# Performance work log

Measured on AMD Instinct MI355X. Metric: run time of the kernel, lower is better.

Reference implementation:

```python
import jax, jax.numpy as jnp
import numpy as np

B, S, D, H = 2, 2048, 768, 12
HD = D // H  # 64
SCALE = jnp.sqrt(jnp.float32(D / H))  # sqrt(head_dim) = 8


def setup_inputs() -> dict:
    key = jax.random.key(0)
    ks = jax.random.split(key, 11)
    s = 1.0 / np.sqrt(D)
    inp = {
        'Q': jax.random.normal(ks[0], (B, S, D), jnp.float32),
        'K': jax.random.normal(ks[1], (B, S, D), jnp.float32),
        'V': jax.random.normal(ks[2], (B, S, D), jnp.float32),
        # True = masked out (causal upper triangle), broadcast over heads
        'mask': jnp.broadcast_to(jnp.triu(jnp.ones((S, S), bool), k=1)[None, None], (B, 1, S, S)),
        'Wq': jax.random.uniform(ks[3], (D, D), jnp.float32, -s, s),
        'bq': jax.random.uniform(ks[4], (D,), jnp.float32, -s, s),
        'Wk': jax.random.uniform(ks[5], (D, D), jnp.float32, -s, s),
        'bk': jax.random.uniform(ks[6], (D,), jnp.float32, -s, s),
        'Wv': jax.random.uniform(ks[7], (D, D), jnp.float32, -s, s),
        'bv': jax.random.uniform(ks[8], (D,), jnp.float32, -s, s),
        'Wo': jax.random.uniform(ks[9], (D, D), jnp.float32, -s, s),
        'bo': jax.random.uniform(ks[10], (D,), jnp.float32, -s, s),
    }
    return inp


def _split_heads(x):  # [B,S,D] -> [B,H,S,HD]
    return x.reshape(B, S, H, HD).transpose(0, 2, 1, 3)


def reference(Q, K, V, mask, Wq, bq, Wk, bk, Wv, bv, Wo, bo):
    q = _split_heads(Q @ Wq.T + bq)
    k = _split_heads(K @ Wk.T + bk)
    v = _split_heads(V @ Wv.T + bv)
    # [B,H,S,S] attention scores
    scores = jnp.einsum('bhqd,bhkd->bhqk', q, k) / SCALE
    scores = jnp.where(mask, jnp.float32(-1e9), scores)
    weights = jax.nn.softmax(scores, axis=-1)
    attn = jnp.einsum('bhqk,bhkd->bhqd', weights, v)
    x = attn.transpose(0, 2, 1, 3).reshape(B, S, D)
    x = x @ Wo.T + bo
    return x, weights
```

## Files before the change

### kernel.cpp

```cpp
#include <hip/hip_runtime.h>

#define S_LEN 2048
#define DMODEL 768
#define NHEAD 12
#define BATCH 2
#define X_ELEMS ((size_t)BATCH * S_LEN * DMODEL)
#define W_ELEMS ((size_t)BATCH * NHEAD * S_LEN * S_LEN)
#define WMAT_ELEMS ((size_t)DMODEL * DMODEL)

typedef __attribute__((ext_vector_type(8))) short bf16x8;
typedef __attribute__((ext_vector_type(4))) float f32x4;

__device__ __forceinline__ unsigned short f2bf(float f) {
    union { float f; unsigned int u; } v; v.f = f;
    unsigned int u = v.u;
    return (unsigned short)((u + 0x7FFFu + ((u >> 16) & 1u)) >> 16);
}

__device__ __forceinline__ bf16x8 pack8(float4 a, float4 b) {
    bf16x8 r;
    r[0] = (short)f2bf(a.x); r[1] = (short)f2bf(a.y);
    r[2] = (short)f2bf(a.z); r[3] = (short)f2bf(a.w);
    r[4] = (short)f2bf(b.x); r[5] = (short)f2bf(b.y);
    r[6] = (short)f2bf(b.z); r[7] = (short)f2bf(b.w);
    return r;
}

__device__ __forceinline__ float rmax16(float v) {
    v = fmaxf(v, __shfl_xor(v, 1));
    v = fmaxf(v, __shfl_xor(v, 2));
    v = fmaxf(v, __shfl_xor(v, 4));
    v = fmaxf(v, __shfl_xor(v, 8));
    return v;
}
__device__ __forceinline__ float rsum16(float v) {
    v += __shfl_xor(v, 1); v += __shfl_xor(v, 2);
    v += __shfl_xor(v, 4); v += __shfl_xor(v, 8);
    return v;
}

struct ConvArgs {
    const float* src[7];
    unsigned short* dst[7];
    int n[7];
};

__global__ __launch_bounds__(256) void convert_kernel(ConvArgs a) {
    int t = blockIdx.y;
    int idx = (blockIdx.x * 256 + threadIdx.x) * 8;
    if (idx >= a.n[t]) return;
    const float4* s = (const float4*)(a.src[t] + idx);
    float4 lo = s[0], hi = s[1];
    *(bf16x8*)(a.dst[t] + idx) = pack8(lo, hi);
}

__global__ __launch_bounds__(256) void gemm_kernel(
    const unsigned short* __restrict__ A, const unsigned short* __restrict__ Bw,
    const float* __restrict__ bias, unsigned short* __restrict__ outb,
    float* __restrict__ outf, int mode, float oscale)
{
    __shared__ unsigned short As[128 * 40];
    __shared__ unsigned short Bs[128 * 40];
    int tid = threadIdx.x;
    int bm = blockIdx.x & 31, bn = blockIdx.x >> 5;
    int m0 = bm * 128, n0 = bn * 128;
    int wid = tid >> 6, l = tid & 63;
    int wr = wid >> 1, wc = wid & 1;
    int lr = l & 15, ks = l >> 4, g = l >> 4;

    int srow = tid >> 1, scg = (tid & 1) * 16;
    const unsigned short* aptr = A + (size_t)(m0 + srow) * DMODEL + scg;
    const unsigned short* bptr = Bw + (size_t)(n0 + srow) * DMODEL + scg;
    unsigned short* adst = &As[srow * 40 + scg];
    unsigned short* bdst = &Bs[srow * 40 + scg];

    bf16x8 ar0 = *(const bf16x8*)aptr, ar1 = *(const bf16x8*)(aptr + 8);
    bf16x8 br0 = *(const bf16x8*)bptr, br1 = *(const bf16x8*)(bptr + 8);

    f32x4 acc[4][4];
#pragma unroll
    for (int mi = 0; mi < 4; ++mi)
#pragma unroll
        for (int ni = 0; ni < 4; ++ni) acc[mi][ni] = (f32x4){0.f, 0.f, 0.f, 0.f};

    for (int kk = 0; kk < 24; ++kk) {
        __syncthreads();
        *(bf16x8*)adst = ar0; *(bf16x8*)(adst + 8) = ar1;
        *(bf16x8*)bdst = br0; *(bf16x8*)(bdst + 8) = br1;
        __syncthreads();
        if (kk < 23) {
            int k0 = (kk + 1) * 32;
            ar0 = *(const bf16x8*)(aptr + k0); ar1 = *(const bf16x8*)(aptr + k0 + 8);
            br0 = *(const bf16x8*)(bptr + k0); br1 = *(const bf16x8*)(bptr + k0 + 8);
        }
        bf16x8 af[4], bf_[4];
#pragma unroll
        for (int mi = 0; mi < 4; ++mi)
            af[mi] = *(const bf16x8*)&As[(wr * 64 + mi * 16 + lr) * 40 + ks * 8];
#pragma unroll
        for (int ni = 0; ni < 4; ++ni)
            bf_[ni] = *(const bf16x8*)&Bs[(wc * 64 + ni * 16 + lr) * 40 + ks * 8];
#pragma unroll
        for (int mi = 0; mi < 4; ++mi)
#pragma unroll
            for (int ni = 0; ni < 4; ++ni)
                acc[mi][ni] = __builtin_amdgcn_mfma_f32_16x16x32_bf16(af[mi], bf_[ni], acc[mi][ni], 0, 0, 0);
    }

#pragma unroll
    for (int mi = 0; mi < 4; ++mi)
#pragma unroll
        for (int ni = 0; ni < 4; ++ni) {
            int ngl = n0 + wc * 64 + ni * 16 + lr;
            float bv = bias[ngl];
            int h = ngl >> 6, d = ngl & 63;
#pragma unroll
            for (int i = 0; i < 4; ++i) {
                int mg = m0 + wr * 64 + mi * 16 + g * 4 + i;
                float val = (acc[mi][ni][i] + bv) * oscale;
                if (mode == 0) {
                    int b = mg >> 11, s = mg & 2047;
                    outb[((size_t)(b * NHEAD + h) * S_LEN + s) * 64 + d] = f2bf(val);
                } else if (mode == 1) {
                    int b = mg >> 11, s = mg & 2047;
                    outb[((size_t)(b * NHEAD + h) * 64 + d) * S_LEN + s] = f2bf(val);
                } else {
                    outf[(size_t)mg * DMODEL + ngl] = val;
                }
            }
        }
}

__global__ __launch_bounds__(256) void zero_upper_kernel(float* __restrict__ wts) {
    int qblk = blockIdx.x >> 5, tcol = blockIdx.x & 31;
    if (tcol <= qblk) return;
    int bh = blockIdx.y;
    int tid = threadIdx.x;
    float4 z = {0.f, 0.f, 0.f, 0.f};
    float* base = wts + ((size_t)bh * S_LEN + qblk * 64) * S_LEN + tcol * 64;
#pragma unroll
    for (int it = 0; it < 4; ++it) {
        int r = it * 16 + (tid >> 4);
        *(float4*)&base[(size_t)r * S_LEN + (tid & 15) * 4] = z;
    }
}

__global__ __launch_bounds__(256) void attn_fused_kernel(
    const unsigned short* __restrict__ qbuf, const unsigned short* __restrict__ kbuf,
    const unsigned short* __restrict__ vTbuf, float* __restrict__ wts,
    unsigned short* __restrict__ abuf)
{
    __shared__ unsigned short kt[64 * 72];
    __shared__ unsigned short vt[64 * 72];
    __shared__ unsigned short pt[128 * 72];
    int tid = threadIdx.x;
    int wid = tid >> 6, l = tid & 63;
    int qblk = 15 - blockIdx.x;
    int bh = blockIdx.y;
    int qb0 = qblk * 128;
    int qr0 = qb0 + wid * 32;
    int lr = l & 15, ks = l >> 4, g = l >> 4;
    int nt = 2 * qblk + 2;
    int tmaxw = (qr0 + 31) >> 6;

    const unsigned short* ksrc = kbuf + (size_t)bh * S_LEN * 64;
    const unsigned short* vsrc = vTbuf + (size_t)bh * 64 * S_LEN;

    bf16x8 qf[2][2];
#pragma unroll
    for (int mi = 0; mi < 2; ++mi) {
        const unsigned short* qp = qbuf + ((size_t)bh * S_LEN + qr0 + mi * 16 + lr) * 64 + ks * 8;
        qf[mi][0] = *(const bf16x8*)qp;
        qf[mi][1] = *(const bf16x8*)(qp + 32);
    }

    int srow = tid >> 2, sgrp = (tid & 3) * 16;
    const unsigned short* kstage = ksrc + (size_t)srow * 64 + sgrp;
    const unsigned short* vstage = vsrc + (size_t)srow * S_LEN + sgrp;
    unsigned short* kdst = &kt[srow * 72 + sgrp];
    unsigned short* vdst = &vt[srow * 72 + sgrp];
    unsigned short* ptw = &pt[(wid * 32) * 72];

    float m[2][4], lsum[2][4];
#pragma unroll
    for (int mi = 0; mi < 2; ++mi)
#pragma unroll
        for (int i = 0; i < 4; ++i) { m[mi][i] = -1e30f; lsum[mi][i] = 0.f; }

    bf16x8 kr0 = *(const bf16x8*)kstage;
    bf16x8 kr1 = *(const bf16x8*)(kstage + 8);
    for (int t = 0; t < nt; ++t) {
        __syncthreads();
        *(bf16x8*)kdst = kr0; *(bf16x8*)(kdst + 8) = kr1;
        __syncthreads();
        if (t + 1 < nt) {
            kr0 = *(const bf16x8*)(kstage + (size_t)(t + 1) * 4096);
            kr1 = *(const bf16x8*)(kstage + (size_t)(t + 1) * 4096 + 8);
        }
        if (t > tmaxw) continue;
        f32x4 accs[2][4];
#pragma unroll
        for (int c = 0; c < 4; ++c) {
            bf16x8 kf0 = *(const bf16x8*)&kt[(c * 16 + lr) * 72 + ks * 8];
            bf16x8 kf1 = *(const bf16x8*)&kt[(c * 16 + lr) * 72 + 32 + ks * 8];
#pragma unroll
            for (int mi = 0; mi < 2; ++mi) {
                f32x4 a = {0.f, 0.f, 0.f, 0.f};
                a = __builtin_amdgcn_mfma_f32_16x16x32_bf16(qf[mi][0], kf0, a, 0, 0, 0);
                a = __builtin_amdgcn_mfma_f32_16x16x32_bf16(qf[mi][1], kf1, a, 0, 0, 0);
                accs[mi][c] = a;
            }
        }
        if (t == tmaxw) {
#pragma unroll
            for (int c = 0; c < 4; ++c) {
                int kcol = t * 64 + c * 16 + lr;
#pragma unroll
                for (int mi = 0; mi < 2; ++mi)
#pragma unroll
                    for (int i = 0; i < 4; ++i)
                        if (kcol > qr0 + mi * 16 + g * 4 + i) accs[mi][c][i] = -1e30f;
            }
        }
#pragma unroll
        for (int mi = 0; mi < 2; ++mi)
#pragma unroll
            for (int i = 0; i < 4; ++i) {
                float a0 = accs[mi][0][i], a1 = accs[mi][1][i];
                float a2 = accs[mi][2][i], a3 = accs[mi][3][i];
                float tm = fmaxf(fmaxf(a0, a1), fmaxf(a2, a3));
                float mn = fmaxf(m[mi][i], tm);
                float ls = lsum[mi][i] * __expf(m[mi][i] - mn);
                float p0 = __expf(a0 - mn); if (a0 < -5e29f) p0 = 0.f;
                float p1 = __expf(a1 - mn); if (a1 < -5e29f) p1 = 0.f;
                float p2 = __expf(a2 - mn); if (a2 < -5e29f) p2 = 0.f;
                float p3 = __expf(a3 - mn); if (a3 < -5e29f) p3 = 0.f;
                lsum[mi][i] = ls + (p0 + p1) + (p2 + p3);
                m[mi][i] = mn;
            }
    }

    float invl[2][4];
#pragma unroll
    for (int mi = 0; mi < 2; ++mi)
#pragma unroll
        for (int i = 0; i < 4; ++i) {
            float mf = rmax16(m[mi][i]);
            float ls = lsum[mi][i] * __expf(m[mi][i] - mf);
            ls = rsum16(ls);
            invl[mi][i] = 1.0f / ls;
            m[mi][i] = mf;
        }

    f32x4 oacc[2][4];
#pragma unroll
    for (int mi = 0; mi < 2; ++mi)
#pragma unroll
        for (int dt = 0; dt < 4; ++dt) oacc[mi][dt] = (f32x4){0.f, 0.f, 0.f, 0.f};

    kr0 = *(const bf16x8*)kstage;
    kr1 = *(const bf16x8*)(kstage + 8);
    bf16x8 vr0 = *(const bf16x8*)vstage;
    bf16x8 vr1 = *(const bf16x8*)(vstage + 8);
    for (int t = 0; t < nt; ++t) {
        __syncthreads();
        *(bf16x8*)kdst = kr0; *(bf16x8*)(kdst + 8) = kr1;
        *(bf16x8*)vdst = vr0; *(bf16x8*)(vdst + 8) = vr1;
        __syncthreads();
        if (t + 1 < nt) {
            kr0 = *(const bf16x8*)(kstage + (size_t)(t + 1) * 4096);
            kr1 = *(const bf16x8*)(kstage + (size_t)(t + 1) * 4096 + 8);
            vr0 = *(const bf16x8*)(vstage + (t + 1) * 64);
            vr1 = *(const bf16x8*)(vstage + (t + 1) * 64 + 8);
        }
        if (t > tmaxw) continue;
        f32x4 accs[2][4];
#pragma unroll
        for (int c = 0; c < 4; ++c) {
            bf16x8 kf0 = *(const bf16x8*)&kt[(c * 16 + lr) * 72 + ks * 8];
            bf16x8 kf1 = *(const bf16x8*)&kt[(c * 16 + lr) * 72 + 32 + ks * 8];
#pragma unroll
            for (int mi = 0; mi < 2; ++mi) {
                f32x4 a = {0.f, 0.f, 0.f, 0.f};
                a = __builtin_amdgcn_mfma_f32_16x16x32_bf16(qf[mi][0], kf0, a, 0, 0, 0);
                a = __builtin_amdgcn_mfma_f32_16x16x32_bf16(qf[mi][1], kf1, a, 0, 0, 0);
                accs[mi][c] = a;
            }
        }
        if (t == tmaxw) {
#pragma unroll
            for (int c = 0; c < 4; ++c) {
                int kcol = t * 64 + c * 16 + lr;
#pragma unroll
                for (int mi = 0; mi < 2; ++mi)
#pragma unroll
                    for (int i = 0; i < 4; ++i)
                        if (kcol > qr0 + mi * 16 + g * 4 + i) accs[mi][c][i] = -1e30f;
            }
        }
#pragma unroll
        for (int c = 0; c < 4; ++c) {
            int kcol = t * 64 + c * 16 + lr;
#pragma unroll
            for (int mi = 0; mi < 2; ++mi)
#pragma unroll
                for (int i = 0; i < 4; ++i) {
                    int qrow = qr0 + mi * 16 + g * 4 + i;
                    float w = __expf(accs[mi][c][i] - m[mi][i]) * invl[mi][i];
                    wts[((size_t)bh * S_LEN + qrow) * S_LEN + kcol] = w;
                    ptw[(mi * 16 + g * 4 + i) * 72 + c * 16 + lr] = f2bf(w);
                }
        }
        bf16x8 pa[2][2];
#pragma unroll
        for (int mi = 0; mi < 2; ++mi) {
            pa[mi][0] = *(const bf16x8*)&ptw[(mi * 16 + lr) * 72 + ks * 8];
            pa[mi][1] = *(const bf16x8*)&ptw[(mi * 16 + lr) * 72 + 32 + ks * 8];
        }
#pragma unroll
        for (int dt = 0; dt < 4; ++dt) {
            bf16x8 vb0 = *(const bf16x8*)&vt[(dt * 16 + lr) * 72 + ks * 8];
            bf16x8 vb1 = *(const bf16x8*)&vt[(dt * 16 + lr) * 72 + 32 + ks * 8];
#pragma unroll
            for (int mi = 0; mi < 2; ++mi) {
                oacc[mi][dt] = __builtin_amdgcn_mfma_f32_16x16x32_bf16(pa[mi][0], vb0, oacc[mi][dt], 0, 0, 0);
                oacc[mi][dt] = __builtin_amdgcn_mfma_f32_16x16x32_bf16(pa[mi][1], vb1, oacc[mi][dt], 0, 0, 0);
            }
        }
    }

    int b = bh / NHEAD, h = bh % NHEAD;
#pragma unroll
    for (int mi = 0; mi < 2; ++mi)
#pragma unroll
        for (int dt = 0; dt < 4; ++dt)
#pragma unroll
            for (int i = 0; i < 4; ++i) {
                int s = qr0 + mi * 16 + g * 4 + i;
                abuf[(((size_t)b * S_LEN + s) * NHEAD + h) * 64 + dt * 16 + lr] = f2bf(oacc[mi][dt][i]);
            }
}

extern "C" void kernel_launch(void* const* d_in, const int* in_sizes, int n_in,
                              void* d_out, int out_size, void* d_ws, size_t ws_size,
                              hipStream_t stream) {
    const float* Q  = (const float*)d_in[0];
    const float* K  = (const float*)d_in[1];
    const float* V  = (const float*)d_in[2];
    const float* Wq = (const float*)d_in[4];
    const float* bq = (const float*)d_in[5];
    const float* Wk = (const float*)d_in[6];
    const float* bk = (const float*)d_in[7];
    const float* Wv = (const float*)d_in[8];
    const float* bv = (const float*)d_in[9];
    const float* Wo = (const float*)d_in[10];
    const float* bo = (const float*)d_in[11];

    float* xout = (float*)d_out;
    float* wts  = xout + X_ELEMS;

    unsigned short* p = (unsigned short*)d_ws;
    unsigned short* Qb   = p; p += X_ELEMS;
    unsigned short* Kb   = p; p += X_ELEMS;
    unsigned short* Vb   = p; p += X_ELEMS;
    unsigned short* Wqb  = p; p += WMAT_ELEMS;
    unsigned short* Wkb  = p; p += WMAT_ELEMS;
    unsigned short* Wvb  = p; p += WMAT_ELEMS;
    unsigned short* Wob  = p; p += WMAT_ELEMS;
    unsigned short* qbuf = p; p += X_ELEMS;
    unsigned short* kbuf = p; p += X_ELEMS;
    unsigned short* vT   = p; p += X_ELEMS;
    unsigned short* abuf = p; p += X_ELEMS;

    ConvArgs ca;
    ca.src[0] = Q;  ca.dst[0] = Qb;  ca.n[0] = (int)X_ELEMS;
    ca.src[1] = K;  ca.dst[1] = Kb;  ca.n[1] = (int)X_ELEMS;
    ca.src[2] = V;  ca.dst[2] = Vb;  ca.n[2] = (int)X_ELEMS;
    ca.src[3] = Wq; ca.dst[3] = Wqb; ca.n[3] = (int)WMAT_ELEMS;
    ca.src[4] = Wk; ca.dst[4] = Wkb; ca.n[4] = (int)WMAT_ELEMS;
    ca.src[5] = Wv; ca.dst[5] = Wvb; ca.n[5] = (int)WMAT_ELEMS;
    ca.src[6] = Wo; ca.dst[6] = Wob; ca.n[6] = (int)WMAT_ELEMS;
    convert_kernel<<<dim3(1536, 7), 256, 0, stream>>>(ca);

    const int GEMM_GRID = 32 * 6;
    gemm_kernel<<<GEMM_GRID, 256, 0, stream>>>(Qb, Wqb, bq, qbuf, nullptr, 0, 0.125f);
    gemm_kernel<<<GEMM_GRID, 256, 0, stream>>>(Kb, Wkb, bk, kbuf, nullptr, 0, 1.0f);
    gemm_kernel<<<GEMM_GRID, 256, 0, stream>>>(Vb, Wvb, bv, vT,   nullptr, 1, 1.0f);

    zero_upper_kernel<<<dim3(32 * 32, 24), 256, 0, stream>>>(wts);

    attn_fused_kernel<<<dim3(16, 24), 256, 0, stream>>>(qbuf, kbuf, vT, wts, abuf);

    gemm_kernel<<<GEMM_GRID, 256, 0, stream>>>(abuf, Wob, bo, nullptr, xout, 2, 1.0f);
}
```

Before: 672.3 us.

## Batch QKV projections, fold zeroing into single-wave attention, use exp2

Merges the three projection GEMMs into one launch indexed by blockIdx.y. The attention kernel becomes a one-wave 32-row block that reads K and V straight from global memory with no LDS staging and no barriers. It also zeroes its own upper-triangle weight tiles, which removes the separate zero kernel. Softmax uses the hardware exp2 instruction, with log2(e) folded into the Q projection scale and -inf masking. Together these cut launch count, sync overhead and idle waves, at the cost of losing K/V reuse across waves and relying more on cache bandwidth.

```diff
diff --git a/kernel.cpp b/kernel.cpp
--- a/kernel.cpp
+++ b/kernel.cpp
@@ -11,6 +11,8 @@
 typedef __attribute__((ext_vector_type(8))) short bf16x8;
 typedef __attribute__((ext_vector_type(4))) float f32x4;
 
+#define NEG_INF (-__builtin_inff())
+
 __device__ __forceinline__ unsigned short f2bf(float f) {
     union { float f; unsigned int u; } v; v.f = f;
     unsigned int u = v.u;
@@ -26,6 +28,10 @@
     return r;
 }
 
+__device__ __forceinline__ float exp2_hw(float x) {
+    float r; asm("v_exp_f32 %0, %1" : "=v"(r) : "v"(x)); return r;
+}
+
 __device__ __forceinline__ float rmax16(float v) {
     v = fmaxf(v, __shfl_xor(v, 1));
     v = fmaxf(v, __shfl_xor(v, 2));
@@ -54,7 +60,7 @@
     *(bf16x8*)(a.dst[t] + idx) = pack8(lo, hi);
 }
 
-__global__ __launch_bounds__(256) void gemm_kernel(
+__device__ __forceinline__ void gemm_core(
     const unsigned short* __restrict__ A, const unsigned short* __restrict__ Bw,
     const float* __restrict__ bias, unsigned short* __restrict__ outb,
     float* __restrict__ outf, int mode, float oscale)
@@ -131,40 +137,44 @@
         }
 }
 
-__global__ __launch_bounds__(256) void zero_upper_kernel(float* __restrict__ wts) {
-    int qblk = blockIdx.x >> 5, tcol = blockIdx.x & 31;
-    if (tcol <= qblk) return;
-    int bh = blockIdx.y;
-    int tid = threadIdx.x;
-    float4 z = {0.f, 0.f, 0.f, 0.f};
-    float* base = wts + ((size_t)bh * S_LEN + qblk * 64) * S_LEN + tcol * 64;
-#pragma unroll
-    for (int it = 0; it < 4; ++it) {
-        int r = it * 16 + (tid >> 4);
-        *(float4*)&base[(size_t)r * S_LEN + (tid & 15) * 4] = z;
-    }
-}
-
-__global__ __launch_bounds__(256) void attn_fused_kernel(
+struct ProjArgs {
+    const unsigned short* A[3];
+    const unsigned short* W[3];
+    const float* bias[3];
+    unsigned short* out[3];
+    int mode[3];
+    float scale[3];
+};
+
+__global__ __launch_bounds__(256) void proj3_kernel(ProjArgs p) {
+    int z = blockIdx.y;
+    gemm_core(p.A[z], p.W[z], p.bias[z], p.out[z], nullptr, p.mode[z], p.scale[z]);
+}
+
+__global__ __launch_bounds__(256) void gemm_kernel(
+    const unsigned short* __restrict__ A, const unsigned short* __restrict__ Bw,
+    const float* __restrict__ bias, unsigned short* __restrict__ outb,
+    float* __restrict__ outf, int mode, float oscale)
+{
+    gemm_core(A, Bw, bias, outb, outf, mode, oscale);
+}
+
+__global__ __launch_bounds__(64) void attn_kernel(
     const unsigned short* __restrict__ qbuf, const unsigned short* __restrict__ kbuf,
     const unsigned short* __restrict__ vTbuf, float* __restrict__ wts,
     unsigned short* __restrict__ abuf)
 {
-    __shared__ unsigned short kt[64 * 72];
-    __shared__ unsigned short vt[64 * 72];
-    __shared__ unsigned short pt[128 * 72];
-    int tid = threadIdx.x;
-    int wid = tid >> 6, l = tid & 63;
-    int qblk = 15 - blockIdx.x;
+    __shared__ unsigned short pt[32 * 72];
+    int l = threadIdx.x;
+    int chunk = 63 - (int)blockIdx.x;
     int bh = blockIdx.y;
-    int qb0 = qblk * 128;
-    int qr0 = qb0 + wid * 32;
+    int qr0 = chunk * 32;
     int lr = l & 15, ks = l >> 4, g = l >> 4;
-    int nt = 2 * qblk + 2;
-    int tmaxw = (qr0 + 31) >> 6;
+    int tdiag = qr0 >> 6;
 
     const unsigned short* ksrc = kbuf + (size_t)bh * S_LEN * 64;
     const unsigned short* vsrc = vTbuf + (size_t)bh * 64 * S_LEN;
+    float* wbh = wts + (size_t)bh * S_LEN * S_LEN;
 
     bf16x8 qf[2][2];
 #pragma unroll
@@ -174,35 +184,19 @@
         qf[mi][1] = *(const bf16x8*)(qp + 32);
     }
 
-    int srow = tid >> 2, sgrp = (tid & 3) * 16;
-    const unsigned short* kstage = ksrc + (size_t)srow * 64 + sgrp;
-    const unsigned short* vstage = vsrc + (size_t)srow * S_LEN + sgrp;
-    unsigned short* kdst = &kt[srow * 72 + sgrp];
-    unsigned short* vdst = &vt[srow * 72 + sgrp];
-    unsigned short* ptw = &pt[(wid * 32) * 72];
-
     float m[2][4], lsum[2][4];
 #pragma unroll
     for (int mi = 0; mi < 2; ++mi)
 #pragma unroll
-        for (int i = 0; i < 4; ++i) { m[mi][i] = -1e30f; lsum[mi][i] = 0.f; }
-
-    bf16x8 kr0 = *(const bf16x8*)kstage;
-    bf16x8 kr1 = *(const bf16x8*)(kstage + 8);
-    for (int t = 0; t < nt; ++t) {
-        __syncthreads();
-        *(bf16x8*)kdst = kr0; *(bf16x8*)(kdst + 8) = kr1;
-        __syncthreads();
-        if (t + 1 < nt) {
-            kr0 = *(const bf16x8*)(kstage + (size_t)(t + 1) * 4096);
-            kr1 = *(const bf16x8*)(kstage + (size_t)(t + 1) * 4096 + 8);
-        }
-        if (t > tmaxw) continue;
+        for (int i = 0; i < 4; ++i) { m[mi][i] = NEG_INF; lsum[mi][i] = 0.f; }
+
+    for (int t = 0; t <= tdiag; ++t) {
         f32x4 accs[2][4];
 #pragma unroll
         for (int c = 0; c < 4; ++c) {
-            bf16x8 kf0 = *(const bf16x8*)&kt[(c * 16 + lr) * 72 + ks * 8];
-            bf16x8 kf1 = *(const bf16x8*)&kt[(c * 16 + lr) * 72 + 32 + ks * 8];
+            const unsigned short* kp = ksrc + (size_t)(t * 64 + c * 16 + lr) * 64 + ks * 8;
+            bf16x8 kf0 = *(const bf16x8*)kp;
+            bf16x8 kf1 = *(const bf16x8*)(kp + 32);
 #pragma unroll
             for (int mi = 0; mi < 2; ++mi) {
                 f32x4 a = {0.f, 0.f, 0.f, 0.f};
@@ -211,7 +205,7 @@
                 accs[mi][c] = a;
             }
         }
-        if (t == tmaxw) {
+        if (t == tdiag) {
 #pragma unroll
             for (int c = 0; c < 4; ++c) {
                 int kcol = t * 64 + c * 16 + lr;
@@ -219,7 +213,7 @@
                 for (int mi = 0; mi < 2; ++mi)
 #pragma unroll
                     for (int i = 0; i < 4; ++i)
-                        if (kcol > qr0 + mi * 16 + g * 4 + i) accs[mi][c][i] = -1e30f;
+                        if (kcol > qr0 + mi * 16 + g * 4 + i) accs[mi][c][i] = NEG_INF;
             }
         }
 #pragma unroll
@@ -229,13 +223,10 @@
                 float a0 = accs[mi][0][i], a1 = accs[mi][1][i];
                 float a2 = accs[mi][2][i], a3 = accs[mi][3][i];
                 float tm = fmaxf(fmaxf(a0, a1), fmaxf(a2, a3));
-                float mn = fmaxf(m[mi][i], tm);
-                float ls = lsum[mi][i] * __expf(m[mi][i] - mn);
-                float p0 = __expf(a0 - mn); if (a0 < -5e29f) p0 = 0.f;
-                float p1 = __expf(a1 - mn); if (a1 < -5e29f) p1 = 0.f;
-                float p2 = __expf(a2 - mn); if (a2 < -5e29f) p2 = 0.f;
-                float p3 = __expf(a3 - mn); if (a3 < -5e29f) p3 = 0.f;
-                lsum[mi][i] = ls + (p0 + p1) + (p2 + p3);
+                float mn = fmaxf(fmaxf(m[mi][i], tm), -1e30f);
+                lsum[mi][i] = lsum[mi][i] * exp2_hw(m[mi][i] - mn)
+                            + exp2_hw(a0 - mn) + exp2_hw(a1 - mn)
+                            + exp2_hw(a2 - mn) + exp2_hw(a3 - mn);
                 m[mi][i] = mn;
             }
     }
@@ -246,8 +237,7 @@
 #pragma unroll
         for (int i = 0; i < 4; ++i) {
             float mf = rmax16(m[mi][i]);
-            float ls = lsum[mi][i] * __expf(m[mi][i] - mf);
-            ls = rsum16(ls);
+            float ls = rsum16(lsum[mi][i] * exp2_hw(m[mi][i] - mf));
             invl[mi][i] = 1.0f / ls;
             m[mi][i] = mf;
         }
@@ -258,27 +248,13 @@
 #pragma unroll
         for (int dt = 0; dt < 4; ++dt) oacc[mi][dt] = (f32x4){0.f, 0.f, 0.f, 0.f};
 
-    kr0 = *(const bf16x8*)kstage;
-    kr1 = *(const bf16x8*)(kstage + 8);
-    bf16x8 vr0 = *(const bf16x8*)vstage;
-    bf16x8 vr1 = *(const bf16x8*)(vstage + 8);
-    for (int t = 0; t < nt; ++t) {
-        __syncthreads();
-        *(bf16x8*)kdst = kr0; *(bf16x8*)(kdst + 8) = kr1;
-        *(bf16x8*)vdst = vr0; *(bf16x8*)(vdst + 8) = vr1;
-        __syncthreads();
-        if (t + 1 < nt) {
-            kr0 = *(const bf16x8*)(kstage + (size_t)(t + 1) * 4096);
-            kr1 = *(const bf16x8*)(kstage + (size_t)(t + 1) * 4096 + 8);
-            vr0 = *(const bf16x8*)(vstage + (t + 1) * 64);
-            vr1 = *(const bf16x8*)(vstage + (t + 1) * 64 + 8);
-        }
-        if (t > tmaxw) continue;
+    for (int t = 0; t <= tdiag; ++t) {
         f32x4 accs[2][4];
 #pragma unroll
         for (int c = 0; c < 4; ++c) {
-            bf16x8 kf0 = *(const bf16x8*)&kt[(c * 16 + lr) * 72 + ks * 8];
-            bf16x8 kf1 = *(const bf16x8*)&kt[(c * 16 + lr) * 72 + 32 + ks * 8];
+            const unsigned short* kp = ksrc + (size_t)(t * 64 + c * 16 + lr) * 64 + ks * 8;
+            bf16x8 kf0 = *(const bf16x8*)kp;
+            bf16x8 kf1 = *(const bf16x8*)(kp + 32);
 #pragma unroll
             for (int mi = 0; mi < 2; ++mi) {
                 f32x4 a = {0.f, 0.f, 0.f, 0.f};
@@ -287,7 +263,7 @@
                 accs[mi][c] = a;
             }
         }
-        if (t == tmaxw) {
+        if (t == tdiag) {
 #pragma unroll
             for (int c = 0; c < 4; ++c) {
                 int kcol = t * 64 + c * 16 + lr;
@@ -295,7 +271,7 @@
                 for (int mi = 0; mi < 2; ++mi)
 #pragma unroll
                     for (int i = 0; i < 4; ++i)
-                        if (kcol > qr0 + mi * 16 + g * 4 + i) accs[mi][c][i] = -1e30f;
+                        if (kcol > qr0 + mi * 16 + g * 4 + i) accs[mi][c][i] = NEG_INF;
             }
         }
 #pragma unroll
@@ -306,21 +282,22 @@
 #pragma unroll
                 for (int i = 0; i < 4; ++i) {
                     int qrow = qr0 + mi * 16 + g * 4 + i;
-                    float w = __expf(accs[mi][c][i] - m[mi][i]) * invl[mi][i];
-                    wts[((size_t)bh * S_LEN + qrow) * S_LEN + kcol] = w;
-                    ptw[(mi * 16 + g * 4 + i) * 72 + c * 16 + lr] = f2bf(w);
+                    float w = exp2_hw(accs[mi][c][i] - m[mi][i]) * invl[mi][i];
+                    wbh[(size_t)qrow * S_LEN + kcol] = w;
+                    pt[(mi * 16 + g * 4 + i) * 72 + c * 16 + lr] = f2bf(w);
                 }
         }
         bf16x8 pa[2][2];
 #pragma unroll
         for (int mi = 0; mi < 2; ++mi) {
-            pa[mi][0] = *(const bf16x8*)&ptw[(mi * 16 + lr) * 72 + ks * 8];
-            pa[mi][1] = *(const bf16x8*)&ptw[(mi * 16 + lr) * 72 + 32 + ks * 8];
+            pa[mi][0] = *(const bf16x8*)&pt[(mi * 16 + lr) * 72 + ks * 8];
+            pa[mi][1] = *(const bf16x8*)&pt[(mi * 16 + lr) * 72 + 32 + ks * 8];
         }
 #pragma unroll
         for (int dt = 0; dt < 4; ++dt) {
-            bf16x8 vb0 = *(const bf16x8*)&vt[(dt * 16 + lr) * 72 + ks * 8];
-            bf16x8 vb1 = *(const bf16x8*)&vt[(dt * 16 + lr) * 72 + 32 + ks * 8];
+            const unsigned short* vp = vsrc + (size_t)(dt * 16 + lr) * S_LEN + t * 64 + ks * 8;
+            bf16x8 vb0 = *(const bf16x8*)vp;
+            bf16x8 vb1 = *(const bf16x8*)(vp + 32);
 #pragma unroll
             for (int mi = 0; mi < 2; ++mi) {
                 oacc[mi][dt] = __builtin_amdgcn_mfma_f32_16x16x32_bf16(pa[mi][0], vb0, oacc[mi][dt], 0, 0, 0);
@@ -339,6 +316,13 @@
                 int s = qr0 + mi * 16 + g * 4 + i;
                 abuf[(((size_t)b * S_LEN + s) * NHEAD + h) * 64 + dt * 16 + lr] = f2bf(oacc[mi][dt][i]);
             }
+
+    float4 z4 = {0.f, 0.f, 0.f, 0.f};
+    for (int t = tdiag + 1; t < 32; ++t) {
+        float* base = wbh + (size_t)(qr0 + (l >> 1)) * S_LEN + t * 64 + (l & 1) * 32;
+#pragma unroll
+        for (int j = 0; j < 8; ++j) *(float4*)(base + j * 4) = z4;
+    }
 }
 
 extern "C" void kernel_launch(void* const* d_in, const int* in_sizes, int n_in,
@@ -382,14 +366,14 @@
     ca.src[6] = Wo; ca.dst[6] = Wob; ca.n[6] = (int)WMAT_ELEMS;
     convert_kernel<<<dim3(1536, 7), 256, 0, stream>>>(ca);
 
-    const int GEMM_GRID = 32 * 6;
-    gemm_kernel<<<GEMM_GRID, 256, 0, stream>>>(Qb, Wqb, bq, qbuf, nullptr, 0, 0.125f);
-    gemm_kernel<<<GEMM_GRID, 256, 0, stream>>>(Kb, Wkb, bk, kbuf, nullptr, 0, 1.0f);
-    gemm_kernel<<<GEMM_GRID, 256, 0, stream>>>(Vb, Wvb, bv, vT,   nullptr, 1, 1.0f);
-
-    zero_upper_kernel<<<dim3(32 * 32, 24), 256, 0, stream>>>(wts);
-
-    attn_fused_kernel<<<dim3(16, 24), 256, 0, stream>>>(qbuf, kbuf, vT, wts, abuf);
-
-    gemm_kernel<<<GEMM_GRID, 256, 0, stream>>>(abuf, Wob, bo, nullptr, xout, 2, 1.0f);
-}
+    const float QSCALE = 0.125f * 1.44269504088896f;
+    ProjArgs pj;
+    pj.A[0] = Qb; pj.W[0] = Wqb; pj.bias[0] = bq; pj.out[0] = qbuf; pj.mode[0] = 0; pj.scale[0] = QSCALE;
+    pj.A[1] = Kb; pj.W[1] = Wkb; pj.bias[1] = bk; pj.out[1] = kbuf; pj.mode[1] = 0; pj.scale[1] = 1.0f;
+    pj.A[2] = Vb; pj.W[2] = Wvb; pj.bias[2] = bv; pj.out[2] = vT;   pj.mode[2] = 1; pj.scale[2] = 1.0f;
+    proj3_kernel<<<dim3(192, 3), 256, 0, stream>>>(pj);
+
+    attn_kernel<<<dim3(64, 24), 64, 0, stream>>>(qbuf, kbuf, vT, wts, abuf);
+
+    gemm_kernel<<<192, 256, 0, stream>>>(abuf, Wob, bo, nullptr, xout, 2, 1.0f);
+}
```

Result: faster. 652.3 us (-3.0%).
